# Kernel optimization log

Hardware: AMD Instinct MI355X
Metric: run time of the kernel (lower is better)

## Reference

```python
import jax, jax.numpy as jnp
import numpy as np

E, K, H, I = 8, 2, 768, 1152  # experts, top_k, hidden, intermediate
T = 4096  # total tokens


def setup_inputs() -> dict:
    key = jax.random.key(0)
    ks = jax.random.split(key, 6)
    return {
        "x": jax.random.normal(ks[0], (T, H), jnp.float32),
        "gate_w": jax.random.normal(ks[1], (E, H), jnp.float32) * 0.02,
        "correction_bias": jnp.zeros((E,), jnp.float32),
        "Wi": jax.random.normal(ks[2], (E, H, 2 * I), jnp.float32) * 0.02,
        "Wo": jax.random.normal(ks[3], (E, I, H), jnp.float32) * 0.02,
        "shared_Wi": jax.random.normal(ks[4], (2 * I, H), jnp.float32) * 0.02,
        "shared_Wo": jax.random.normal(ks[5], (H, I), jnp.float32) * 0.02,
    }


def reference(x, gate_w, correction_bias, Wi, Wo, shared_Wi, shared_Wo):
    # ---- shared SwiGLU expert (dropout=0 in eval) ----
    sh = x @ shared_Wi.T                      # (T, 2I)
    s_in, s_gate = sh[:, :I], sh[:, I:]
    shared_out = (jax.nn.silu(s_in) * s_gate) @ shared_Wo.T  # (T, H)

    # ---- sigmoid top-k router with bias correction ----
    logits = jax.nn.sigmoid(x @ gate_w.T)     # (T, E)
    sel = logits + correction_bias
    _, indices = jax.lax.top_k(sel, K)        # (T, K)
    weights = jnp.take_along_axis(logits, indices, axis=-1)  # bias-free scores
    weights = weights / jnp.sum(weights, axis=-1, keepdims=True)

    # combine weight per (expert, token): cw[e, t] = sum_k weights[t,k]*[indices[t,k]==e]
    one_hot = jax.nn.one_hot(indices, E, dtype=x.dtype)      # (T, K, E)
    cw = jnp.einsum("tke,tk->et", one_hot, weights)          # (E, T)

    # ---- experts: SwiGLU per expert, weighted scatter-combine ----
    h = jnp.einsum("th,ehf->etf", x, Wi)      # (E, T, 2I)
    proj, gate = h[..., :I], h[..., I:]
    act = jax.nn.silu(gate) * proj            # (E, T, I)
    act = act * cw[:, :, None]                # fold combine weights before Wo
    expert_out = jnp.einsum("eti,eih->th", act, Wo)          # (T, H)

    return expert_out + shared_out
```

## Files before the change

### kernel.cpp

```cpp
#include <hip/hip_runtime.h>
#include <stdint.h>

#define E_  8
#define H_  768
#define I_  1152
#define T_  4096
#define F2_ (2*I_)

typedef unsigned short u16;
typedef __attribute__((ext_vector_type(8))) __bf16 bf16x8;
typedef __attribute__((ext_vector_type(4))) float floatx4;

typedef const void __attribute__((address_space(1))) as1_void;
typedef void __attribute__((address_space(3))) as3_void;

__device__ __forceinline__ void gld16(void* lds, const void* g) {
  __builtin_amdgcn_global_load_lds((as1_void*)g, (as3_void*)lds, 16, 0, 0);
}

__device__ __forceinline__ u16 f2bf(float f) {
  union { float f; unsigned int i; } v; v.f = f;
  unsigned int r = v.i + 0x7FFF + ((v.i >> 16) & 1);
  return (u16)(r >> 16);
}

__global__ void convert_two(const float* __restrict__ s1, u16* __restrict__ d1, int n1,
                            const float* __restrict__ s2, u16* __restrict__ d2) {
  int i = (blockIdx.x * 256 + threadIdx.x) * 4;
  const float* s; u16* d;
  if (i < n1) { s = s1 + i; d = d1 + i; }
  else        { s = s2 + (i - n1); d = d2 + (i - n1); }
  float4 v = *(const float4*)s;
  ushort4 u;
  u.x = f2bf(v.x); u.y = f2bf(v.y); u.z = f2bf(v.z); u.w = f2bf(v.w);
  *(ushort4*)d = u;
}

__global__ void transpose_f2b(const float* __restrict__ src, u16* __restrict__ dst,
                              int R, int C) {
  __shared__ u16 tile[64][65];
  const float* s = src + (long)blockIdx.z * R * C;
  u16*         d = dst + (long)blockIdx.z * R * C;
  int r0 = blockIdx.y * 64, c0 = blockIdx.x * 64;
  int tx = threadIdx.x, ty = threadIdx.y;
  #pragma unroll
  for (int k = 0; k < 64; k += 8)
    tile[ty + k][tx] = f2bf(s[(long)(r0 + ty + k) * C + (c0 + tx)]);
  __syncthreads();
  #pragma unroll
  for (int k = 0; k < 64; k += 8)
    d[(long)(c0 + ty + k) * R + (r0 + tx)] = tile[tx][ty + k];
}

__global__ void gate_kernel(const float* __restrict__ x, const float* __restrict__ gw,
                            const float* __restrict__ bias,
                            int* __restrict__ top2e, float* __restrict__ top2w,
                            u16* __restrict__ xb) {
  int t    = blockIdx.x * 4 + (threadIdx.x >> 6);
  int lane = threadIdx.x & 63;
  float acc[E_];
  #pragma unroll
  for (int e = 0; e < E_; e++) acc[e] = 0.f;
  #pragma unroll
  for (int k = lane; k < H_; k += 64) {
    float xv = x[(long)t * H_ + k];
    xb[(long)t * H_ + k] = f2bf(xv);
    #pragma unroll
    for (int e = 0; e < E_; e++) acc[e] += xv * gw[e * H_ + k];
  }
  #pragma unroll
  for (int e = 0; e < E_; e++) {
    #pragma unroll
    for (int s = 32; s > 0; s >>= 1) acc[e] += __shfl_xor(acc[e], s);
  }
  if (lane == 0) {
    float logits[E_], sel[E_];
    #pragma unroll
    for (int e = 0; e < E_; e++) {
      logits[e] = 1.f / (1.f + expf(-acc[e]));
      sel[e]    = logits[e] + bias[e];
    }
    int i0 = 0;
    #pragma unroll
    for (int e = 1; e < E_; e++) if (sel[e] > sel[i0]) i0 = e;
    int i1 = (i0 == 0) ? 1 : 0;
    #pragma unroll
    for (int e = 0; e < E_; e++) if (e != i0 && sel[e] > sel[i1]) i1 = e;
    float w0 = logits[i0], w1 = logits[i1], s = w0 + w1;
    top2e[t * 2 + 0] = i0;  top2w[t * 2 + 0] = w0 / s;
    top2e[t * 2 + 1] = i1;  top2w[t * 2 + 1] = w1 / s;
  }
}

__global__ void build_lists(const int* __restrict__ top2e, const float* __restrict__ top2w,
                            int* __restrict__ counts, int* __restrict__ offs,
                            int* __restrict__ list, float* __restrict__ wlist,
                            int* __restrict__ pos) {
  __shared__ int lds_cnt[E_];
  __shared__ int lds_off[E_];
  int wv = threadIdx.x >> 6, lane = threadIdx.x & 63;

  int c = 0;
  for (int s = lane; s < 2 * T_; s += 64)
    if (top2e[s] == wv) c++;
  #pragma unroll
  for (int s = 32; s > 0; s >>= 1) c += __shfl_xor(c, s);
  if (lane == 0) lds_cnt[wv] = c;
  __syncthreads();
  if (threadIdx.x == 0) {
    int s = 0;
    #pragma unroll
    for (int e = 0; e < E_; e++) {
      lds_off[e] = s;
      counts[e]  = lds_cnt[e];
      offs[e]    = s;
      s += lds_cnt[e];
    }
    counts[8] = T_;
    offs[8]   = 2 * T_;
  }
  __syncthreads();

  int base = lds_off[wv];
  unsigned long long lt = (lane == 63) ? ~0ull >> 1 : ((1ull << lane) - 1);
  for (int s0 = 0; s0 < 2 * T_; s0 += 64) {
    int s = s0 + lane;
    bool m = (top2e[s] == wv);
    unsigned long long mask = __ballot(m);
    if (m) {
      int p = base + __popcll(mask & lt);
      list[p]  = s >> 1;
      wlist[p] = top2w[s];
      pos[s]   = p;
    }
    base += __popcll(mask);
  }
  for (int t = threadIdx.x; t < T_; t += 512) {
    list[2 * T_ + t]  = t;
    wlist[2 * T_ + t] = 1.f;
  }
}

#define PP1 168
__global__ __launch_bounds__(256, 2)
void gemm_act_all(const u16* __restrict__ A, const u16* __restrict__ WiT,
                  const u16* __restrict__ sWib, u16* __restrict__ act,
                  const int* __restrict__ list, const float* __restrict__ wlist,
                  const int* __restrict__ counts, const int* __restrict__ offsets) {
  __shared__ __align__(16) u16 As[128 * 32];
  __shared__ __align__(16) u16 Bs[2][64 * 32];

  int id = blockIdx.x;
  int y  = id / PP1, p = id - y * PP1;
  if (p >= 162) return;
  int z = p / 18, xblk = p - z * 18;

  int cnt = counts[z], off = offsets[z];
  int row0 = y * 128;
  if (row0 >= cnt) return;
  const u16* B = (z == 8) ? sWib : (WiT + (long)z * F2_ * H_);
  int n0 = xblk * 64;

  int tid  = threadIdx.x;
  int lane = tid & 63, wv = tid >> 6;
  int wr   = wv >> 1, wc = wv & 1;
  int half = lane & 15, quad = lane >> 4;

  int kc  = (tid & 3) * 8;
  int jl0 = row0 + (tid >> 2);
  int jl1 = jl0 + 64;
  int rr0 = min(jl0, cnt - 1), rr1 = min(jl1, cnt - 1);
  int t0  = list[off + rr0];
  int t1  = list[off + rr1];
  const u16* ap0 = A + (long)t0 * H_ + kc;
  const u16* ap1 = A + (long)t1 * H_ + kc;
  int nloc = tid >> 2;
  const u16* bp0 = B + (long)(n0 + nloc) * H_ + kc;
  const u16* bp1 = B + (long)(I_ + n0 + nloc) * H_ + kc;
  u16* asd0 = As + tid * 8;
  u16* asd1 = As + (tid + 256) * 8;
  u16* bsd0 = Bs[0] + tid * 8;
  u16* bsd1 = Bs[1] + tid * 8;

  floatx4 acc[2][4][2];
  #pragma unroll
  for (int q = 0; q < 2; q++)
    #pragma unroll
    for (int i = 0; i < 4; i++)
      #pragma unroll
      for (int j = 0; j < 2; j++) acc[q][i][j] = (floatx4)0.f;

  for (int k0 = 0; k0 < H_; k0 += 32) {
    if (k0) __syncthreads();
    gld16(asd0, ap0 + k0);
    gld16(asd1, ap1 + k0);
    gld16(bsd0, bp0 + k0);
    gld16(bsd1, bp1 + k0);
    __syncthreads();
    bf16x8 a[4], bq[2][2];
    #pragma unroll
    for (int i = 0; i < 4; i++)
      a[i] = *(const bf16x8*)(As + (wr * 64 + i * 16 + half) * 32 + quad * 8);
    #pragma unroll
    for (int q = 0; q < 2; q++)
      #pragma unroll
      for (int j = 0; j < 2; j++)
        bq[q][j] = *(const bf16x8*)(Bs[q] + (wc * 32 + j * 16 + half) * 32 + quad * 8);
    #pragma unroll
    for (int i = 0; i < 4; i++)
      #pragma unroll
      for (int q = 0; q < 2; q++)
        #pragma unroll
        for (int j = 0; j < 2; j++)
          acc[q][i][j] = __builtin_amdgcn_mfma_f32_16x16x32_bf16(a[i], bq[q][j], acc[q][i][j], 0, 0, 0);
  }

  bool sh = (z == 8);
  #pragma unroll
  for (int i = 0; i < 4; i++) {
    #pragma unroll
    for (int r = 0; r < 4; r++) {
      int g = row0 + wr * 64 + i * 16 + quad * 4 + r;
      if (g < cnt) {
        float w = wlist[off + g];
        #pragma unroll
        for (int j = 0; j < 2; j++) {
          float va = acc[0][i][j][r];
          float vb = acc[1][i][j][r];
          float zz = sh ? va : vb;
          float o  = sh ? vb : va;
          float sg = zz / (1.f + expf(-zz));
          float v  = sg * o * w;
          int col  = n0 + wc * 32 + j * 16 + half;
          act[(long)(off + g) * I_ + col] = f2bf(v);
        }
      }
    }
  }
}

#define PP2 56
__global__ __launch_bounds__(256, 2)
void gemm_out_all(const u16* __restrict__ A, const u16* __restrict__ WoT,
                  const u16* __restrict__ sWob, float* __restrict__ out,
                  float* __restrict__ eobuf,
                  const int* __restrict__ counts, const int* __restrict__ offsets) {
  __shared__ __align__(16) u16 As[128 * 32];
  __shared__ __align__(16) u16 Bs[128 * 32];

  int id = blockIdx.x;
  int y  = id / PP2, p = id - y * PP2;
  if (p >= 54) return;
  int z = p / 6, xblk = p - z * 6;

  int cnt = counts[z], off = offsets[z];
  int row0 = y * 128;
  if (row0 >= cnt) return;
  const u16* B = (z == 8) ? sWob : (WoT + (long)z * H_ * I_);
  int n0 = xblk * 128;

  int tid  = threadIdx.x;
  int lane = tid & 63, wv = tid >> 6;
  int wr   = wv >> 1, wc = wv & 1;
  int half = lane & 15, quad = lane >> 4;

  int kc  = (tid & 3) * 8;
  int jl0 = row0 + (tid >> 2);
  int jl1 = jl0 + 64;
  long ar0 = off + min(jl0, cnt - 1);
  long ar1 = off + min(jl1, cnt - 1);
  const u16* ap0 = A + ar0 * I_ + kc;
  const u16* ap1 = A + ar1 * I_ + kc;
  int nl0 = n0 + (tid >> 2);
  const u16* bp0 = B + (long)nl0 * I_ + kc;
  const u16* bp1 = B + (long)(nl0 + 64) * I_ + kc;
  u16* asd0 = As + tid * 8;
  u16* asd1 = As + (tid + 256) * 8;
  u16* bsd0 = Bs + tid * 8;
  u16* bsd1 = Bs + (tid + 256) * 8;

  floatx4 acc[4][4];
  #pragma unroll
  for (int i = 0; i < 4; i++)
    #pragma unroll
    for (int j = 0; j < 4; j++) acc[i][j] = (floatx4)0.f;

  for (int k0 = 0; k0 < I_; k0 += 32) {
    if (k0) __syncthreads();
    gld16(asd0, ap0 + k0);
    gld16(asd1, ap1 + k0);
    gld16(bsd0, bp0 + k0);
    gld16(bsd1, bp1 + k0);
    __syncthreads();
    bf16x8 a[4], b[4];
    #pragma unroll
    for (int i = 0; i < 4; i++)
      a[i] = *(const bf16x8*)(As + (wr * 64 + i * 16 + half) * 32 + quad * 8);
    #pragma unroll
    for (int j = 0; j < 4; j++)
      b[j] = *(const bf16x8*)(Bs + (wc * 64 + j * 16 + half) * 32 + quad * 8);
    #pragma unroll
    for (int i = 0; i < 4; i++)
      #pragma unroll
      for (int j = 0; j < 4; j++)
        acc[i][j] = __builtin_amdgcn_mfma_f32_16x16x32_bf16(a[i], b[j], acc[i][j], 0, 0, 0);
  }

  bool sh = (z == 8);
  #pragma unroll
  for (int i = 0; i < 4; i++) {
    #pragma unroll
    for (int r = 0; r < 4; r++) {
      int g = row0 + wr * 64 + i * 16 + quad * 4 + r;
      if (g < cnt) {
        float* orow = sh ? (out + (long)g * H_) : (eobuf + (long)(off + g) * H_);
        #pragma unroll
        for (int j = 0; j < 4; j++) {
          int col = n0 + wc * 64 + j * 16 + half;
          orow[col] = acc[i][j][r];
        }
      }
    }
  }
}

__global__ void final_reduce(float* __restrict__ out, const float* __restrict__ eobuf,
                             const int* __restrict__ pos) {
  int gid = blockIdx.x * 256 + threadIdx.x;
  int t = gid / (H_ / 4), c = (gid % (H_ / 4)) * 4;
  int p0 = pos[t * 2], p1 = pos[t * 2 + 1];
  float4 a = *(const float4*)(out   + (long)t  * H_ + c);
  float4 b = *(const float4*)(eobuf + (long)p0 * H_ + c);
  float4 d = *(const float4*)(eobuf + (long)p1 * H_ + c);
  a.x += b.x + d.x; a.y += b.y + d.y; a.z += b.z + d.z; a.w += b.w + d.w;
  *(float4*)(out + (long)t * H_ + c) = a;
}

extern "C" void kernel_launch(void* const* d_in, const int* in_sizes, int n_in,
                              void* d_out, int out_size, void* d_ws, size_t ws_size,
                              hipStream_t stream) {
  const float* x      = (const float*)d_in[0];
  const float* gate_w = (const float*)d_in[1];
  const float* bias   = (const float*)d_in[2];
  const float* Wi     = (const float*)d_in[3];
  const float* Wo     = (const float*)d_in[4];
  const float* sWi    = (const float*)d_in[5];
  const float* sWo    = (const float*)d_in[6];
  float* out          = (float*)d_out;

  char* ws = (char*)d_ws;
  size_t o = 0;
  auto alloc = [&](size_t bytes) -> void* {
    o = (o + 255) & ~(size_t)255;
    void* p = ws + o;
    o += bytes;
    return p;
  };
  u16*   xb    = (u16*)  alloc((size_t)T_ * H_ * 2);
  u16*   sWib  = (u16*)  alloc((size_t)F2_ * H_ * 2);
  u16*   sWob  = (u16*)  alloc((size_t)H_ * I_ * 2);
  u16*   WiT   = (u16*)  alloc((size_t)E_ * F2_ * H_ * 2);
  u16*   WoT   = (u16*)  alloc((size_t)E_ * H_ * I_ * 2);
  u16*   act   = (u16*)  alloc((size_t)3 * T_ * I_ * 2);
  int*   top2e = (int*)  alloc((size_t)T_ * 2 * 4);
  float* top2w = (float*)alloc((size_t)T_ * 2 * 4);
  int*   count = (int*)  alloc(9 * 4);
  int*   offs  = (int*)  alloc(9 * 4);
  int*   list  = (int*)  alloc((size_t)3 * T_ * 4);
  float* wlist = (float*)alloc((size_t)3 * T_ * 4);
  int*   pos   = (int*)  alloc((size_t)2 * T_ * 4);
  float* eobuf = (float*)WiT;

  gate_kernel<<<T_ / 4, 256, 0, stream>>>(x, gate_w, bias, top2e, top2w, xb);
  build_lists<<<1, 512, 0, stream>>>(top2e, top2w, count, offs, list, wlist, pos);

  convert_two<<<(F2_ * H_ + H_ * I_) / 1024, 256, 0, stream>>>(
      sWi, sWib, F2_ * H_, sWo, sWob);
  transpose_f2b<<<dim3(F2_ / 64, H_ / 64, E_), dim3(64, 8), 0, stream>>>(Wi, WiT, H_, F2_);
  transpose_f2b<<<dim3(H_ / 64, I_ / 64, E_), dim3(64, 8), 0, stream>>>(Wo, WoT, I_, H_);

  gemm_act_all<<<32 * PP1, 256, 0, stream>>>(xb, WiT, sWib, act, list, wlist, count, offs);
  gemm_out_all<<<32 * PP2, 256, 0, stream>>>(act, WoT, sWob, out, eobuf, count, offs);
  final_reduce<<<(T_ * (H_ / 4)) / 256, 256, 0, stream>>>(out, eobuf, pos);
}
```

Before: 342.2 us.

## Double K-tile to 64 with XOR-swizzled LDS, vectorize gate, parallelize list build

Both grouped GEMMs now stage 64-wide K slices per barrier instead of 32, which halves the number of syncs. They use an XOR swizzle on the 16-byte LDS chunks to avoid bank conflicts on the MFMA fragment reads, at the cost of doubled LDS per block. The gate kernel switches to float4 loads and packed bf16 stores. List building is spread over 8 blocks, one per expert, with each wave scanning a quarter of the assignments instead of running in a single block. Each block recomputes the global counts to derive offsets.

```diff
diff --git a/kernel.cpp b/kernel.cpp
--- a/kernel.cpp
+++ b/kernel.cpp
@@ -62,11 +62,17 @@
   #pragma unroll
   for (int e = 0; e < E_; e++) acc[e] = 0.f;
   #pragma unroll
-  for (int k = lane; k < H_; k += 64) {
-    float xv = x[(long)t * H_ + k];
-    xb[(long)t * H_ + k] = f2bf(xv);
-    #pragma unroll
-    for (int e = 0; e < E_; e++) acc[e] += xv * gw[e * H_ + k];
+  for (int i = 0; i < H_ / 256; i++) {
+    int c = i * 256 + lane * 4;
+    float4 xv = *(const float4*)(x + (long)t * H_ + c);
+    ushort4 u;
+    u.x = f2bf(xv.x); u.y = f2bf(xv.y); u.z = f2bf(xv.z); u.w = f2bf(xv.w);
+    *(ushort4*)(xb + (long)t * H_ + c) = u;
+    #pragma unroll
+    for (int e = 0; e < E_; e++) {
+      float4 g = *(const float4*)(gw + e * H_ + c);
+      acc[e] += xv.x * g.x + xv.y * g.y + xv.z * g.z + xv.w * g.w;
+    }
   }
   #pragma unroll
   for (int e = 0; e < E_; e++) {
@@ -96,36 +102,55 @@
                             int* __restrict__ counts, int* __restrict__ offs,
                             int* __restrict__ list, float* __restrict__ wlist,
                             int* __restrict__ pos) {
-  __shared__ int lds_cnt[E_];
-  __shared__ int lds_off[E_];
-  int wv = threadIdx.x >> 6, lane = threadIdx.x & 63;
-
-  int c = 0;
-  for (int s = lane; s < 2 * T_; s += 64)
-    if (top2e[s] == wv) c++;
-  #pragma unroll
-  for (int s = 32; s > 0; s >>= 1) c += __shfl_xor(c, s);
-  if (lane == 0) lds_cnt[wv] = c;
+  __shared__ int scnt[4][E_];
+  __shared__ int sq[4];
+  __shared__ int soffs[E_];
+  int e = blockIdx.x;
+  int tid = threadIdx.x, w = tid >> 6, lane = tid & 63;
+  const int Q = (2 * T_) / 4;
+
+  int c8[E_];
+  #pragma unroll
+  for (int q = 0; q < E_; q++) c8[q] = 0;
+  for (int i = tid; i < 2 * T_; i += 256) {
+    int v = top2e[i];
+    #pragma unroll
+    for (int q = 0; q < E_; q++) c8[q] += (v == q);
+  }
+  int qstart = w * Q;
+  int ce = 0;
+  for (int i = qstart + lane; i < qstart + Q; i += 64) ce += (top2e[i] == e);
+  #pragma unroll
+  for (int q = 0; q < E_; q++)
+    #pragma unroll
+    for (int s = 32; s > 0; s >>= 1) c8[q] += __shfl_xor(c8[q], s);
+  #pragma unroll
+  for (int s = 32; s > 0; s >>= 1) ce += __shfl_xor(ce, s);
+  if (lane == 0) {
+    #pragma unroll
+    for (int q = 0; q < E_; q++) scnt[w][q] = c8[q];
+    sq[w] = ce;
+  }
   __syncthreads();
-  if (threadIdx.x == 0) {
+  if (tid == 0) {
     int s = 0;
     #pragma unroll
-    for (int e = 0; e < E_; e++) {
-      lds_off[e] = s;
-      counts[e]  = lds_cnt[e];
-      offs[e]    = s;
-      s += lds_cnt[e];
-    }
-    counts[8] = T_;
-    offs[8]   = 2 * T_;
+    for (int q = 0; q < E_; q++) {
+      int tot = scnt[0][q] + scnt[1][q] + scnt[2][q] + scnt[3][q];
+      soffs[q] = s;
+      if (e == 0) { counts[q] = tot; offs[q] = s; }
+      s += tot;
+    }
+    if (e == 0) { counts[8] = T_; offs[8] = 2 * T_; }
   }
   __syncthreads();
-
-  int base = lds_off[wv];
-  unsigned long long lt = (lane == 63) ? ~0ull >> 1 : ((1ull << lane) - 1);
-  for (int s0 = 0; s0 < 2 * T_; s0 += 64) {
-    int s = s0 + lane;
-    bool m = (top2e[s] == wv);
+  int base = soffs[e];
+  #pragma unroll
+  for (int w2 = 0; w2 < 4; w2++) if (w2 < w) base += sq[w2];
+  unsigned long long lt = (lane == 63) ? (~0ull >> 1) : ((1ull << lane) - 1);
+  for (int i0 = qstart; i0 < qstart + Q; i0 += 64) {
+    int s = i0 + lane;
+    bool m = (top2e[s] == e);
     unsigned long long mask = __ballot(m);
     if (m) {
       int p = base + __popcll(mask & lt);
@@ -135,7 +160,7 @@
     }
     base += __popcll(mask);
   }
-  for (int t = threadIdx.x; t < T_; t += 512) {
+  for (int t = e * (T_ / 8) + tid; t < (e + 1) * (T_ / 8); t += 256) {
     list[2 * T_ + t]  = t;
     wlist[2 * T_ + t] = 1.f;
   }
@@ -147,8 +172,8 @@
                   const u16* __restrict__ sWib, u16* __restrict__ act,
                   const int* __restrict__ list, const float* __restrict__ wlist,
                   const int* __restrict__ counts, const int* __restrict__ offsets) {
-  __shared__ __align__(16) u16 As[128 * 32];
-  __shared__ __align__(16) u16 Bs[2][64 * 32];
+  __shared__ __align__(16) u16 As[128 * 64];
+  __shared__ __align__(16) u16 Bs[2][64 * 64];
 
   int id = blockIdx.x;
   int y  = id / PP1, p = id - y * PP1;
@@ -166,21 +191,20 @@
   int wr   = wv >> 1, wc = wv & 1;
   int half = lane & 15, quad = lane >> 4;
 
-  int kc  = (tid & 3) * 8;
-  int jl0 = row0 + (tid >> 2);
-  int jl1 = jl0 + 64;
-  int rr0 = min(jl0, cnt - 1), rr1 = min(jl1, cnt - 1);
-  int t0  = list[off + rr0];
-  int t1  = list[off + rr1];
-  const u16* ap0 = A + (long)t0 * H_ + kc;
-  const u16* ap1 = A + (long)t1 * H_ + kc;
-  int nloc = tid >> 2;
-  const u16* bp0 = B + (long)(n0 + nloc) * H_ + kc;
-  const u16* bp1 = B + (long)(I_ + n0 + nloc) * H_ + kc;
-  u16* asd0 = As + tid * 8;
-  u16* asd1 = As + (tid + 256) * 8;
-  u16* bsd0 = Bs[0] + tid * 8;
-  u16* bsd1 = Bs[1] + tid * 8;
+  int rA  = tid >> 3;
+  int lc8 = ((tid & 7) ^ (rA & 7)) * 8;
+  const u16* ap[4];
+  #pragma unroll
+  for (int n = 0; n < 4; n++) {
+    int rr = min(row0 + rA + n * 32, cnt - 1);
+    ap[n] = A + (long)list[off + rr] * H_ + lc8;
+  }
+  const u16* bp[2][2];
+  #pragma unroll
+  for (int h = 0; h < 2; h++)
+    #pragma unroll
+    for (int m = 0; m < 2; m++)
+      bp[h][m] = B + (long)(h * I_ + n0 + m * 32 + rA) * H_ + lc8;
 
   floatx4 acc[2][4][2];
   #pragma unroll
@@ -190,29 +214,35 @@
       #pragma unroll
       for (int j = 0; j < 2; j++) acc[q][i][j] = (floatx4)0.f;
 
-  for (int k0 = 0; k0 < H_; k0 += 32) {
+  for (int k0 = 0; k0 < H_; k0 += 64) {
     if (k0) __syncthreads();
-    gld16(asd0, ap0 + k0);
-    gld16(asd1, ap1 + k0);
-    gld16(bsd0, bp0 + k0);
-    gld16(bsd1, bp1 + k0);
+    #pragma unroll
+    for (int n = 0; n < 4; n++) gld16(As + (n * 256 + tid) * 8, ap[n] + k0);
+    #pragma unroll
+    for (int h = 0; h < 2; h++)
+      #pragma unroll
+      for (int m = 0; m < 2; m++) gld16(Bs[h] + (m * 256 + tid) * 8, bp[h][m] + k0);
     __syncthreads();
-    bf16x8 a[4], bq[2][2];
-    #pragma unroll
-    for (int i = 0; i < 4; i++)
-      a[i] = *(const bf16x8*)(As + (wr * 64 + i * 16 + half) * 32 + quad * 8);
-    #pragma unroll
-    for (int q = 0; q < 2; q++)
-      #pragma unroll
-      for (int j = 0; j < 2; j++)
-        bq[q][j] = *(const bf16x8*)(Bs[q] + (wc * 32 + j * 16 + half) * 32 + quad * 8);
-    #pragma unroll
-    for (int i = 0; i < 4; i++)
+    #pragma unroll
+    for (int kk = 0; kk < 2; kk++) {
+      int cs = ((kk * 4 + quad) ^ (half & 7)) * 8;
+      bf16x8 a[4], bq[2][2];
+      #pragma unroll
+      for (int i = 0; i < 4; i++)
+        a[i] = *(const bf16x8*)(As + (wr * 64 + i * 16 + half) * 64 + cs);
       #pragma unroll
       for (int q = 0; q < 2; q++)
         #pragma unroll
         for (int j = 0; j < 2; j++)
-          acc[q][i][j] = __builtin_amdgcn_mfma_f32_16x16x32_bf16(a[i], bq[q][j], acc[q][i][j], 0, 0, 0);
+          bq[q][j] = *(const bf16x8*)(Bs[q] + (wc * 32 + j * 16 + half) * 64 + cs);
+      #pragma unroll
+      for (int i = 0; i < 4; i++)
+        #pragma unroll
+        for (int q = 0; q < 2; q++)
+          #pragma unroll
+          for (int j = 0; j < 2; j++)
+            acc[q][i][j] = __builtin_amdgcn_mfma_f32_16x16x32_bf16(a[i], bq[q][j], acc[q][i][j], 0, 0, 0);
+    }
   }
 
   bool sh = (z == 8);
@@ -245,8 +275,8 @@
                   const u16* __restrict__ sWob, float* __restrict__ out,
                   float* __restrict__ eobuf,
                   const int* __restrict__ counts, const int* __restrict__ offsets) {
-  __shared__ __align__(16) u16 As[128 * 32];
-  __shared__ __align__(16) u16 Bs[128 * 32];
+  __shared__ __align__(16) u16 As[128 * 64];
+  __shared__ __align__(16) u16 Bs[128 * 64];
 
   int id = blockIdx.x;
   int y  = id / PP2, p = id - y * PP2;
@@ -264,20 +294,18 @@
   int wr   = wv >> 1, wc = wv & 1;
   int half = lane & 15, quad = lane >> 4;
 
-  int kc  = (tid & 3) * 8;
-  int jl0 = row0 + (tid >> 2);
-  int jl1 = jl0 + 64;
-  long ar0 = off + min(jl0, cnt - 1);
-  long ar1 = off + min(jl1, cnt - 1);
-  const u16* ap0 = A + ar0 * I_ + kc;
-  const u16* ap1 = A + ar1 * I_ + kc;
-  int nl0 = n0 + (tid >> 2);
-  const u16* bp0 = B + (long)nl0 * I_ + kc;
-  const u16* bp1 = B + (long)(nl0 + 64) * I_ + kc;
-  u16* asd0 = As + tid * 8;
-  u16* asd1 = As + (tid + 256) * 8;
-  u16* bsd0 = Bs + tid * 8;
-  u16* bsd1 = Bs + (tid + 256) * 8;
+  int rA  = tid >> 3;
+  int lc8 = ((tid & 7) ^ (rA & 7)) * 8;
+  const u16* ap[4];
+  #pragma unroll
+  for (int n = 0; n < 4; n++) {
+    long rr = off + min(row0 + rA + n * 32, cnt - 1);
+    ap[n] = A + rr * I_ + lc8;
+  }
+  const u16* bp[4];
+  #pragma unroll
+  for (int m = 0; m < 4; m++)
+    bp[m] = B + (long)(n0 + m * 32 + rA) * I_ + lc8;
 
   floatx4 acc[4][4];
   #pragma unroll
@@ -285,25 +313,29 @@
     #pragma unroll
     for (int j = 0; j < 4; j++) acc[i][j] = (floatx4)0.f;
 
-  for (int k0 = 0; k0 < I_; k0 += 32) {
+  for (int k0 = 0; k0 < I_; k0 += 64) {
     if (k0) __syncthreads();
-    gld16(asd0, ap0 + k0);
-    gld16(asd1, ap1 + k0);
-    gld16(bsd0, bp0 + k0);
-    gld16(bsd1, bp1 + k0);
+    #pragma unroll
+    for (int n = 0; n < 4; n++) gld16(As + (n * 256 + tid) * 8, ap[n] + k0);
+    #pragma unroll
+    for (int m = 0; m < 4; m++) gld16(Bs + (m * 256 + tid) * 8, bp[m] + k0);
     __syncthreads();
-    bf16x8 a[4], b[4];
-    #pragma unroll
-    for (int i = 0; i < 4; i++)
-      a[i] = *(const bf16x8*)(As + (wr * 64 + i * 16 + half) * 32 + quad * 8);
-    #pragma unroll
-    for (int j = 0; j < 4; j++)
-      b[j] = *(const bf16x8*)(Bs + (wc * 64 + j * 16 + half) * 32 + quad * 8);
-    #pragma unroll
-    for (int i = 0; i < 4; i++)
+    #pragma unroll
+    for (int kk = 0; kk < 2; kk++) {
+      int cs = ((kk * 4 + quad) ^ (half & 7)) * 8;
+      bf16x8 a[4], b[4];
+      #pragma unroll
+      for (int i = 0; i < 4; i++)
+        a[i] = *(const bf16x8*)(As + (wr * 64 + i * 16 + half) * 64 + cs);
       #pragma unroll
       for (int j = 0; j < 4; j++)
-        acc[i][j] = __builtin_amdgcn_mfma_f32_16x16x32_bf16(a[i], b[j], acc[i][j], 0, 0, 0);
+        b[j] = *(const bf16x8*)(Bs + (wc * 64 + j * 16 + half) * 64 + cs);
+      #pragma unroll
+      for (int i = 0; i < 4; i++)
+        #pragma unroll
+        for (int j = 0; j < 4; j++)
+          acc[i][j] = __builtin_amdgcn_mfma_f32_16x16x32_bf16(a[i], b[j], acc[i][j], 0, 0, 0);
+    }
   }
 
   bool sh = (z == 8);
@@ -372,7 +404,7 @@
   float* eobuf = (float*)WiT;
 
   gate_kernel<<<T_ / 4, 256, 0, stream>>>(x, gate_w, bias, top2e, top2w, xb);
-  build_lists<<<1, 512, 0, stream>>>(top2e, top2w, count, offs, list, wlist, pos);
+  build_lists<<<E_, 256, 0, stream>>>(top2e, top2w, count, offs, list, wlist, pos);
 
   convert_two<<<(F2_ * H_ + H_ * I_) / 1024, 256, 0, stream>>>(
       sWi, sWib, F2_ * H_, sWo, sWob);
```

New measurement: 294.5 us. 1.16x faster.
